# Kernel tuning notes

Hardware: AMD Instinct MI355X
Metric: run time of the kernel (lower is better)

The kernel has to match this reference:

```python
import jax, jax.numpy as jnp
import numpy as np

B, S, D = 16, 1024, 768
H = 12
HD = D // H  # 64


def setup_inputs() -> dict:
    key = jax.random.key(0)
    k1, k2, k3 = jax.random.split(key, 3)
    scale_in = 1.0 / np.sqrt(D)
    return {
        "x": jax.random.normal(k1, (B, S, D), dtype=jnp.float32),
        "w_qkv": jax.random.normal(k2, (3 * D, D), dtype=jnp.float32) * scale_in,
        "b_qkv": jnp.zeros((3 * D,), dtype=jnp.float32),
        "w_proj": jax.random.normal(k3, (D, D), dtype=jnp.float32) * scale_in,
        "b_proj": jnp.zeros((D,), dtype=jnp.float32),
    }


def reference(x, w_qkv, b_qkv, w_proj, b_proj):
    b, s, d = x.shape
    scale = HD ** -0.5
    # qkv projection: [B,S,3D] -> [3,B,H,S,HD]
    qkv = x @ w_qkv.T + b_qkv
    qkv = qkv.reshape(b, s, 3, H, HD).transpose(2, 0, 3, 1, 4)
    q, k, v = qkv[0], qkv[1], qkv[2]
    q = q * scale
    attn = jnp.einsum("bhqd,bhkd->bhqk", q, k)  # [B,H,S,S]
    attn = jax.nn.softmax(attn, axis=-1)
    # attn_dropout is identity in eval mode
    z = jnp.einsum("bhqk,bhkd->bhqd", attn, v)
    z = z.transpose(0, 2, 1, 3).reshape(b, s, d)
    return z @ w_proj.T + b_proj
```

## Files before the change

kernel.cpp:

```cpp
#include <hip/hip_runtime.h>
#include <hip/hip_bf16.h>
#include <cstdint>
#include <cstddef>

typedef __attribute__((ext_vector_type(8))) short short8;
typedef __attribute__((ext_vector_type(4))) float floatx4;
typedef __attribute__((ext_vector_type(16))) float floatx16;
typedef unsigned short u16;

__device__ __forceinline__ u16 f2bf(float f) {
  unsigned u = __float_as_uint(f);
  u += 0x7FFFu + ((u >> 16) & 1u);
  return (u16)(u >> 16);
}

__device__ __forceinline__ unsigned cvt_pk_bf16(float a, float b) {
  unsigned r;
  asm("v_cvt_pk_bf16_f32 %0, %1, %2" : "=v"(r) : "v"(a), "v"(b));
  return r;
}

__device__ __forceinline__ float fexp2(float x) {
#if __has_builtin(__builtin_amdgcn_exp2f)
  return __builtin_amdgcn_exp2f(x);
#else
  float r;
  asm("v_exp_f32 %0, %1\n\ts_nop 1" : "=v"(r) : "v"(x));
  return r;
#endif
}

__device__ __forceinline__ float frcp(float x) {
#if __has_builtin(__builtin_amdgcn_rcpf)
  return __builtin_amdgcn_rcpf(x);
#else
  float r;
  asm("v_rcp_f32 %0, %1\n\ts_nop 1" : "=v"(r) : "v"(x));
  return r;
#endif
}

__device__ __forceinline__ void gload16(const u16* g, u16* l) {
  __builtin_amdgcn_global_load_lds(
      (const __attribute__((address_space(1))) void*)g,
      (__attribute__((address_space(3))) void*)l, 16, 0, 0);
}

__global__ void cvt3_kernel(const float* __restrict__ a, u16* __restrict__ oa, int na4,
                            const float* __restrict__ b, u16* __restrict__ ob, int nb4,
                            const float* __restrict__ c, u16* __restrict__ oc, int nc4) {
  int i = blockIdx.x * blockDim.x + threadIdx.x;
  int stride = gridDim.x * blockDim.x;
  int ntot = na4 + nb4 + nc4;
  for (int idx = i; idx < ntot; idx += stride) {
    const float* src; u16* dst; int j = idx;
    if (j < na4)            { src = a; dst = oa; }
    else if (j < na4 + nb4) { src = b; dst = ob; j -= na4; }
    else                    { src = c; dst = oc; j -= na4 + nb4; }
    float4 v = reinterpret_cast<const float4*>(src)[j];
    ushort4 o = make_ushort4(f2bf(v.x), f2bf(v.y), f2bf(v.z), f2bf(v.w));
    reinterpret_cast<ushort4*>(dst)[j] = o;
  }
}

template<bool OUTF32>
__global__ __launch_bounds__(256) void gemm_bt128(
    const u16* __restrict__ A, const u16* __restrict__ B,
    const float* __restrict__ bias, void* __restrict__ Cout,
    int M, int N, int K, int qcols, float qscale)
{
  __shared__ u16 As[128 * 32];
  __shared__ u16 Bs[128 * 32];
  const int tid = threadIdx.x;
  const int lane = tid & 63, w = tid >> 6;
  const int l15 = lane & 15, lhi = lane >> 4;
  const int wm = w >> 1, wn = w & 1;

  const int mblocks = M >> 7;
  const int nb = N >> 7;
  const int bid = blockIdx.x;
  const int xcd = bid & 7;
  const int local = bid >> 3;
  const int mpx = mblocks >> 3;
  const int m0 = (xcd * mpx + local / nb) << 7;
  const int n0 = (local % nb) << 7;

  const int srow = tid >> 2;
  const int scol = (tid & 3) * 8;
  const u16* aptr = A + (size_t)(m0 + srow) * K + scol;
  const u16* bptr = B + (size_t)(n0 + srow) * K + scol;
  const size_t r64 = (size_t)64 * K;

  u16* asd0 = As + w * 512;
  u16* asd1 = As + 2048 + w * 512;
  u16* bsd0 = Bs + w * 512;
  u16* bsd1 = Bs + 2048 + w * 512;

  floatx4 acc[4][4] = {};

  for (int k0 = 0; k0 < K; k0 += 32) {
    __syncthreads();
    gload16(aptr + k0,       asd0);
    gload16(aptr + k0 + r64, asd1);
    gload16(bptr + k0,       bsd0);
    gload16(bptr + k0 + r64, bsd1);
    __syncthreads();

    short8 af[4], bf[4];
#pragma unroll
    for (int i = 0; i < 4; ++i) {
      af[i] = *reinterpret_cast<const short8*>(&As[(wm * 64 + i * 16 + l15) * 32 + lhi * 8]);
      bf[i] = *reinterpret_cast<const short8*>(&Bs[(wn * 64 + i * 16 + l15) * 32 + lhi * 8]);
    }
#pragma unroll
    for (int i = 0; i < 4; ++i)
#pragma unroll
      for (int j = 0; j < 4; ++j)
        acc[i][j] = __builtin_amdgcn_mfma_f32_16x16x32_bf16(af[i], bf[j], acc[i][j], 0, 0, 0);
  }

#pragma unroll
  for (int i = 0; i < 4; ++i)
#pragma unroll
    for (int j = 0; j < 4; ++j) {
      int row = m0 + wm * 64 + i * 16 + lhi * 4;
      int col = n0 + wn * 64 + j * 16 + l15;
      float bv = bias[col];
      float sc = (col < qcols) ? qscale : 1.0f;
#pragma unroll
      for (int r = 0; r < 4; ++r) {
        float v = (acc[i][j][r] + bv) * sc;
        if (OUTF32) reinterpret_cast<float*>(Cout)[(size_t)(row + r) * N + col] = v;
        else        reinterpret_cast<u16*>(Cout)[(size_t)(row + r) * N + col] = f2bf(v);
      }
    }
}

__global__ __launch_bounds__(256) void vtrans_kernel(
    const u16* __restrict__ qkv, u16* __restrict__ vt)
{
  __shared__ u16 T[64][72];
  const int idx = blockIdx.x;
  const int st = idx & 15;
  const int bh = idx >> 4;
  const int b = bh / 12, h = bh % 12;
  const int t = threadIdx.x;
  const int r2 = t >> 3, c8 = (t & 7) * 8;

  const u16* src = qkv + ((size_t)(b * 1024 + st * 64)) * 2304 + 1536 + h * 64;
#pragma unroll
  for (int rr = 0; rr < 2; ++rr) {
    int s = rr * 32 + r2;
    short8 v = *reinterpret_cast<const short8*>(src + (size_t)s * 2304 + c8);
    *reinterpret_cast<short8*>(&T[s][c8]) = v;
  }
  __syncthreads();
  u16* dst = vt + (size_t)bh * 64 * 1024 + st * 64;
#pragma unroll
  for (int rr = 0; rr < 2; ++rr) {
    int d = rr * 32 + r2;
    short8 o;
#pragma unroll
    for (int j = 0; j < 8; ++j) o[j] = T[c8 + j][d];
    *reinterpret_cast<short8*>(dst + (size_t)d * 1024 + c8) = o;
  }
}

__global__ __launch_bounds__(512) void attn8_kernel(
    const u16* __restrict__ qkv, const u16* __restrict__ vt, u16* __restrict__ z)
{
  constexpr int LDK = 72;
  __shared__ u16 Ks[64 * LDK];
  __shared__ u16 Vs[64 * LDK];

  const int tid = threadIdx.x;
  const int lane = tid & 63, w = tid >> 6;
  const int l31 = lane & 31, hi = lane >> 5;

  const int idx = blockIdx.x;
  const int head = idx % 192;
  const int qt   = idx / 192;
  const int b = head / 12, h = head % 12;

  const size_t rowbase = (size_t)b * 1024;
  const u16* Qp  = qkv + rowbase * 2304 + h * 64;
  const u16* Kp  = Qp + 768;
  const u16* Vtp = vt + (size_t)head * 64 * 1024;

  const int q0 = qt * 256 + w * 32;

  short8 qf[4];
#pragma unroll
  for (int c = 0; c < 4; ++c)
    qf[c] = *reinterpret_cast<const short8*>(
        Qp + (size_t)(q0 + l31) * 2304 + c * 16 + hi * 8);

  union { unsigned u[4]; short8 v; } ONE;
#pragma unroll
  for (int i = 0; i < 4; ++i) ONE.u[i] = 0x3F803F80u;
  const short8 ones = ONE.v;

  const int srow = tid >> 3, scol = (tid & 7) * 8;

  const u16* kstage = Kp + (size_t)srow * 2304 + scol;
  const u16* vstage = Vtp + (size_t)srow * 1024 + scol;
  constexpr size_t KADV = (size_t)64 * 2304;
  constexpr size_t VADV = 64;

  u16* const ksw = &Ks[srow * LDK + scol];
  u16* const vsw = &Vs[srow * LDK + scol];
  const u16* const ks0 = &Ks[l31 * LDK + hi * 8];
  const u16* const ks1 = ks0 + 32 * LDK;
  const u16* const vs0 = &Vs[l31 * LDK + hi * 8];
  const u16* const vs1 = vs0 + 32 * LDK;

  short8 kvr = *reinterpret_cast<const short8*>(kstage);
  short8 vvr = *reinterpret_cast<const short8*>(vstage);
  kstage += KADV; vstage += VADV;

  floatx16 oacc0 = {}, oacc1 = {}, lacc = {};

  for (int kt = 0; kt < 16; ++kt) {
    __syncthreads();
    *reinterpret_cast<short8*>(ksw) = kvr;
    *reinterpret_cast<short8*>(vsw) = vvr;
    __syncthreads();

    if (kt < 15) {
      kvr = *reinterpret_cast<const short8*>(kstage);
      vvr = *reinterpret_cast<const short8*>(vstage);
      kstage += KADV; vstage += VADV;
    }

    floatx16 s0 = {}, s1 = {};
    __builtin_amdgcn_s_setprio(1);
#pragma unroll
    for (int c = 0; c < 4; ++c) {
      short8 kf0 = *reinterpret_cast<const short8*>(ks0 + c * 16);
      short8 kf1 = *reinterpret_cast<const short8*>(ks1 + c * 16);
      s0 = __builtin_amdgcn_mfma_f32_32x32x16_bf16(kf0, qf[c], s0, 0, 0, 0);
      s1 = __builtin_amdgcn_mfma_f32_32x32x16_bf16(kf1, qf[c], s1, 0, 0, 0);
    }
    __builtin_amdgcn_s_setprio(0);

#pragma unroll
    for (int r = 0; r < 16; ++r) {
      s0[r] = fexp2(s0[r]);
      s1[r] = fexp2(s1[r]);
    }

    short8 pa[4];
#pragma unroll
    for (int c = 0; c < 4; ++c) {
      const floatx16& sv = (c >> 1) ? s1 : s0;
      const int B0 = (c & 1) * 8, B1 = B0 + 4;
      unsigned x0 = cvt_pk_bf16(sv[B0],     sv[B0 + 1]);
      unsigned x1 = cvt_pk_bf16(sv[B0 + 2], sv[B0 + 3]);
      unsigned y0 = cvt_pk_bf16(sv[B1],     sv[B1 + 1]);
      unsigned y1 = cvt_pk_bf16(sv[B1 + 2], sv[B1 + 3]);
      asm("s_nop 1\n\tv_permlane32_swap_b32 %0, %1" : "+v"(x0), "+v"(y0));
      asm("s_nop 1\n\tv_permlane32_swap_b32 %0, %1" : "+v"(x1), "+v"(y1));
      union { unsigned u[4]; short8 v; } P;
      P.u[0] = x0; P.u[1] = x1; P.u[2] = y0; P.u[3] = y1;
      pa[c] = P.v;
    }

    __builtin_amdgcn_s_setprio(1);
#pragma unroll
    for (int c = 0; c < 4; ++c) {
      short8 vf0 = *reinterpret_cast<const short8*>(vs0 + c * 16);
      short8 vf1 = *reinterpret_cast<const short8*>(vs1 + c * 16);
      oacc0 = __builtin_amdgcn_mfma_f32_32x32x16_bf16(pa[c], vf0, oacc0, 0, 0, 0);
      oacc1 = __builtin_amdgcn_mfma_f32_32x32x16_bf16(pa[c], vf1, oacc1, 0, 0, 0);
      lacc  = __builtin_amdgcn_mfma_f32_32x32x16_bf16(pa[c], ones, lacc, 0, 0, 0);
    }
    __builtin_amdgcn_s_setprio(0);
  }

#pragma unroll
  for (int r = 0; r < 16; ++r) {
    int q = (r & 3) + 8 * (r >> 2) + 4 * hi;
    float li = frcp(lacc[r]);
    size_t orow = (rowbase + q0 + q) * (size_t)768 + h * 64;
    z[orow + l31]      = f2bf(oacc0[r] * li);
    z[orow + 32 + l31] = f2bf(oacc1[r] * li);
  }
}

extern "C" void kernel_launch(void* const* d_in, const int* in_sizes, int n_in,
                              void* d_out, int out_size, void* d_ws, size_t ws_size,
                              hipStream_t stream) {
  (void)in_sizes; (void)n_in; (void)out_size; (void)ws_size;
  const float* x      = (const float*)d_in[0];
  const float* w_qkv  = (const float*)d_in[1];
  const float* b_qkv  = (const float*)d_in[2];
  const float* w_proj = (const float*)d_in[3];
  const float* b_proj = (const float*)d_in[4];
  float* out = (float*)d_out;

  const int BS = 16 * 1024;
  const int D = 768, N3 = 2304;
  const float QSC = 0.180336880f;

  u16* xb  = (u16*)d_ws;
  u16* wqb = xb  + (size_t)BS * D;
  u16* wpb = wqb + (size_t)N3 * D;
  u16* qkv = wpb + (size_t)D * D;
  u16* zb  = qkv + (size_t)BS * N3;
  u16* vtb = xb;

  cvt3_kernel<<<2048, 256, 0, stream>>>(x, xb, BS * D / 4,
                                        w_qkv, wqb, N3 * D / 4,
                                        w_proj, wpb, D * D / 4);

  gemm_bt128<false><<<(BS / 128) * (N3 / 128), 256, 0, stream>>>(
      xb, wqb, b_qkv, qkv, BS, N3, D, 768, QSC);
  vtrans_kernel<<<192 * 16, 256, 0, stream>>>(qkv, vtb);
  attn8_kernel<<<192 * 4, 512, 0, stream>>>(qkv, vtb, zb);
  gemm_bt128<true><<<(BS / 128) * (D / 128), 256, 0, stream>>>(
      zb, wpb, b_proj, out, BS, D, D, 0, 1.0f);
}
```

Baseline: 220.5 us.

## Double-buffer LDS tiles in bf16 GEMM to overlap global loads with MFMA

The QKV/projection GEMM kernel now allocates two LDS buffers per operand and prefetches the next K-slice via direct global-to-LDS loads while MFMAs consume the current slice. This replaces the two barriers per iteration with a single vmcnt wait plus barrier at the end of each step. It also raises wave priority around the MFMA block. LDS use doubles, which may lower occupancy, and correctness depends on the one-barrier scheme protecting buffer reuse.

```diff
diff --git a/kernel.cpp b/kernel.cpp
--- a/kernel.cpp
+++ b/kernel.cpp
@@ -69,8 +69,8 @@
     const float* __restrict__ bias, void* __restrict__ Cout,
     int M, int N, int K, int qcols, float qscale)
 {
-  __shared__ u16 As[128 * 32];
-  __shared__ u16 Bs[128 * 32];
+  __shared__ u16 As[2 * 128 * 32];
+  __shared__ u16 Bs[2 * 128 * 32];
   const int tid = threadIdx.x;
   const int lane = tid & 63, w = tid >> 6;
   const int l15 = lane & 15, lhi = lane >> 4;
@@ -91,32 +91,52 @@
   const u16* bptr = B + (size_t)(n0 + srow) * K + scol;
   const size_t r64 = (size_t)64 * K;
 
-  u16* asd0 = As + w * 512;
-  u16* asd1 = As + 2048 + w * 512;
-  u16* bsd0 = Bs + w * 512;
-  u16* bsd1 = Bs + 2048 + w * 512;
+  const int ksteps = K >> 5;
+  const int wbase = w * 512;
 
   floatx4 acc[4][4] = {};
 
-  for (int k0 = 0; k0 < K; k0 += 32) {
-    __syncthreads();
-    gload16(aptr + k0,       asd0);
-    gload16(aptr + k0 + r64, asd1);
-    gload16(bptr + k0,       bsd0);
-    gload16(bptr + k0 + r64, bsd1);
-    __syncthreads();
-
+  gload16(aptr,       As + wbase);
+  gload16(aptr + r64, As + 2048 + wbase);
+  gload16(bptr,       Bs + wbase);
+  gload16(bptr + r64, Bs + 2048 + wbase);
+  asm volatile("s_waitcnt vmcnt(0)" ::: "memory");
+  __builtin_amdgcn_s_barrier();
+  __builtin_amdgcn_sched_barrier(0);
+
+  int cur = 0;
+  for (int t = 0; t < ksteps; ++t) {
+    const int nxt = cur ^ 1;
+    if (t + 1 < ksteps) {
+      const int k1 = (t + 1) << 5;
+      gload16(aptr + k1,       As + nxt * 4096 + wbase);
+      gload16(aptr + k1 + r64, As + nxt * 4096 + 2048 + wbase);
+      gload16(bptr + k1,       Bs + nxt * 4096 + wbase);
+      gload16(bptr + k1 + r64, Bs + nxt * 4096 + 2048 + wbase);
+    }
+
+    const u16* Ab = As + cur * 4096;
+    const u16* Bb = Bs + cur * 4096;
     short8 af[4], bf[4];
 #pragma unroll
     for (int i = 0; i < 4; ++i) {
-      af[i] = *reinterpret_cast<const short8*>(&As[(wm * 64 + i * 16 + l15) * 32 + lhi * 8]);
-      bf[i] = *reinterpret_cast<const short8*>(&Bs[(wn * 64 + i * 16 + l15) * 32 + lhi * 8]);
-    }
+      af[i] = *reinterpret_cast<const short8*>(&Ab[(wm * 64 + i * 16 + l15) * 32 + lhi * 8]);
+      bf[i] = *reinterpret_cast<const short8*>(&Bb[(wn * 64 + i * 16 + l15) * 32 + lhi * 8]);
+    }
+    __builtin_amdgcn_s_setprio(1);
 #pragma unroll
     for (int i = 0; i < 4; ++i)
 #pragma unroll
       for (int j = 0; j < 4; ++j)
         acc[i][j] = __builtin_amdgcn_mfma_f32_16x16x32_bf16(af[i], bf[j], acc[i][j], 0, 0, 0);
+    __builtin_amdgcn_s_setprio(0);
+
+    if (t + 1 < ksteps) {
+      asm volatile("s_waitcnt vmcnt(0)" ::: "memory");
+      __builtin_amdgcn_s_barrier();
+      __builtin_amdgcn_sched_barrier(0);
+    }
+    cur = nxt;
   }
 
 #pragma unroll
```

New measurement: 214.5 us. -2.7%, faster.
